# Kernel optimization log

Measured on AMD Instinct MI355X. Metric: run time of the kernel, lower is better.

Reference implementation:

```python
import jax, jax.numpy as jnp
import numpy as np

DIM = 1024
HEADS = 16
EPS = 1e-5


def layer_norm(x, gamma, beta):
    mu = jnp.mean(x, axis=-1, keepdims=True)
    var = jnp.mean(jnp.square(x - mu), axis=-1, keepdims=True)
    return (x - mu) * jax.lax.rsqrt(var + EPS) * gamma + beta


def setup_inputs() -> dict:
    key = jax.random.key(0)
    ks = jax.random.split(key, 9)
    B, Nq, Nk = 8, 1024, 1024
    s = 1.0 / np.sqrt(DIM)
    return {
        "x": jax.random.normal(ks[0], (B, Nq, DIM), jnp.float32),
        "context": jax.random.normal(ks[1], (B, Nk, DIM), jnp.float32),
        "relative_position_bias": jax.random.normal(ks[2], (HEADS, Nq, Nk), jnp.float32),
        "Wq": jax.random.normal(ks[3], (DIM, DIM), jnp.float32) * s,
        "Wk": jax.random.normal(ks[4], (DIM, DIM), jnp.float32) * s,
        "Wv": jax.random.normal(ks[5], (DIM, DIM), jnp.float32) * s,
        "Wo": jax.random.normal(ks[6], (DIM, DIM), jnp.float32) * s,
        "bo": jnp.zeros((DIM,), jnp.float32),
        "gamma": jnp.ones((DIM,), jnp.float32),
        "beta": jnp.zeros((DIM,), jnp.float32),
    }


def reference(x, context, relative_position_bias, Wq, Wk, Wv, Wo, bo, gamma, beta):
    h = HEADS
    d = DIM // h
    scale = d ** -0.5
    xn = layer_norm(x, gamma, beta)
    cn = layer_norm(context, gamma, beta)
    B, Nq, _ = x.shape
    Nk = context.shape[1]
    # b n (h d) -> b h n d
    q = (xn @ Wq).reshape(B, Nq, h, d).transpose(0, 2, 1, 3)
    k = (cn @ Wk).reshape(B, Nk, h, d).transpose(0, 2, 1, 3)
    v = (cn @ Wv).reshape(B, Nk, h, d).transpose(0, 2, 1, 3)
    scores = jnp.einsum('bhid,bhjd->bhij', q, k) * scale
    scores = scores + relative_position_bias[None]
    attn = jax.nn.softmax(scores, axis=-1)
    out = jnp.einsum('bhij,bhjd->bhid', attn, v)
    out = out.transpose(0, 2, 1, 3).reshape(B, Nq, h * d)
    return out @ Wo + bo
```

## Files before the change

### kernel.cpp

```cpp
#include <hip/hip_runtime.h>
#include <hip/hip_bf16.h>
#include <stdint.h>

#define DIM   1024
#define HEADS 16
#define HD    64
#define NB    8
#define NTOK  1024
#define MROWS (NB*NTOK)

typedef __attribute__((ext_vector_type(8))) _Float16 f16x8;
typedef __attribute__((ext_vector_type(4))) _Float16 f16x4;
typedef __attribute__((ext_vector_type(4))) float    f32x4;

typedef unsigned int uint_as1 __attribute__((address_space(1)));
typedef unsigned int uint_as3 __attribute__((address_space(3)));

__device__ __forceinline__ void gload16(const void* g, void* l) {
    __builtin_amdgcn_global_load_lds((const uint_as1*)g, (uint_as3*)l, 16, 0, 0);
}

__device__ __forceinline__ unsigned pkrtz(float a, float b) {
    auto h = __builtin_amdgcn_cvt_pkrtz(a, b);
    return __builtin_bit_cast(unsigned, h);
}

__global__ __launch_bounds__(256) void ln_kernel(const float* __restrict__ x,
                                                 const float* __restrict__ ctx,
                                                 const float* __restrict__ gamma,
                                                 const float* __restrict__ beta,
                                                 _Float16* __restrict__ xn,
                                                 _Float16* __restrict__ cn) {
    int row = blockIdx.x;
    const float* src; _Float16* dst;
    if (row < MROWS) { src = x + (size_t)row * DIM;          dst = xn + (size_t)row * DIM; }
    else             { int r = row - MROWS;
                       src = ctx + (size_t)r * DIM;          dst = cn + (size_t)r * DIM; }
    int t = threadIdx.x;
    float4 v = *(const float4*)(src + t * 4);
    float s  = v.x + v.y + v.z + v.w;
    float s2 = v.x*v.x + v.y*v.y + v.z*v.z + v.w*v.w;
    #pragma unroll
    for (int o = 32; o; o >>= 1) { s += __shfl_xor(s, o, 64); s2 += __shfl_xor(s2, o, 64); }
    __shared__ float red[8];
    int w = t >> 6, l = t & 63;
    if (l == 0) { red[w] = s; red[4 + w] = s2; }
    __syncthreads();
    s  = red[0] + red[1] + red[2] + red[3];
    s2 = red[4] + red[5] + red[6] + red[7];
    float mu   = s * (1.0f / DIM);
    float rstd = rsqrtf(s2 * (1.0f / DIM) - mu * mu + 1e-5f);
    float4 g  = *(const float4*)(gamma + t * 4);
    float4 bb = *(const float4*)(beta  + t * 4);
    f16x4 o;
    o[0] = (_Float16)((v.x - mu) * rstd * g.x + bb.x);
    o[1] = (_Float16)((v.y - mu) * rstd * g.y + bb.y);
    o[2] = (_Float16)((v.z - mu) * rstd * g.z + bb.z);
    o[3] = (_Float16)((v.w - mu) * rstd * g.w + bb.w);
    *(f16x4*)(dst + t * 4) = o;
}

__global__ __launch_bounds__(256) void wtrans_kernel(const float* __restrict__ Wq, const float* __restrict__ Wk,
                                                     const float* __restrict__ Wv, const float* __restrict__ Wo,
                                                     _Float16* __restrict__ Tq, _Float16* __restrict__ Tk,
                                                     _Float16* __restrict__ Tv, _Float16* __restrict__ To) {
    __shared__ float tile[32][33];
    int m = blockIdx.z;
    const float* W = (m == 0) ? Wq : (m == 1) ? Wk : (m == 2) ? Wv : Wo;
    _Float16*    T = (m == 0) ? Tq : (m == 1) ? Tk : (m == 2) ? Tv : To;
    int j0 = blockIdx.x * 32, k0 = blockIdx.y * 32;
    int tx = threadIdx.x, ty = threadIdx.y;
    #pragma unroll
    for (int i = 0; i < 4; i++) tile[ty + i*8][tx] = W[(size_t)(k0 + ty + i*8) * DIM + j0 + tx];
    __syncthreads();
    #pragma unroll
    for (int i = 0; i < 4; i++) T[(size_t)(j0 + ty + i*8) * DIM + k0 + tx] = (_Float16)tile[tx][ty + i*8];
}

template<int MODE>
__global__ __launch_bounds__(256) void gemm_bt(const _Float16* __restrict__ A,
                                               const _Float16* __restrict__ BT,
                                               void* __restrict__ Cout,
                                               const float* __restrict__ bias) {
    __shared__ _Float16 As[128 * 32];
    __shared__ _Float16 Bs[128 * 32];
    const int K = DIM;
    int m0 = blockIdx.x * 128, n0 = blockIdx.y * 128;
    int t = threadIdx.x, w = t >> 6, l = t & 63;
    int wr = w >> 1, wc = w & 1, ln = l & 15, qtr = l >> 4;
    f32x4 acc[4][4] = {};
    int srow = t >> 2, scol = (t & 3) * 8;
    const _Float16* Ag = A  + (size_t)(m0 + srow) * K + scol;
    const _Float16* Bg = BT + (size_t)(n0 + srow) * K + scol;
    _Float16* Al = &As[(w * 16) * 32];
    _Float16* Bl = &Bs[(w * 16) * 32];
    for (int kt = 0; kt < K; kt += 32) {
        gload16(Ag,                    Al);
        gload16(Ag + (size_t)64 * K,   Al + 64 * 32);
        gload16(Bg,                    Bl);
        gload16(Bg + (size_t)64 * K,   Bl + 64 * 32);
        Ag += 32; Bg += 32;
        __syncthreads();
        f16x8 af[4], bfr[4];
        #pragma unroll
        for (int r = 0; r < 4; r++) af[r]  = *(const f16x8*)&As[(wr * 64 + r * 16 + ln) * 32 + qtr * 8];
        #pragma unroll
        for (int c = 0; c < 4; c++) bfr[c] = *(const f16x8*)&Bs[(wc * 64 + c * 16 + ln) * 32 + qtr * 8];
        #pragma unroll
        for (int r = 0; r < 4; r++)
            #pragma unroll
            for (int c = 0; c < 4; c++)
                acc[r][c] = __builtin_amdgcn_mfma_f32_16x16x32_f16(af[r], bfr[c], acc[r][c], 0, 0, 0);
        __syncthreads();
    }
    #pragma unroll
    for (int r = 0; r < 4; r++)
        #pragma unroll
        for (int c = 0; c < 4; c++) {
            int gn = n0 + wc * 64 + c * 16 + ln;
            #pragma unroll
            for (int q = 0; q < 4; q++) {
                int gm = m0 + wr * 64 + r * 16 + qtr * 4 + q;
                float v = acc[r][c][q];
                if constexpr (MODE == 0) {
                    int b = gm >> 10, n = gm & 1023, h = gn >> 6, d = gn & 63;
                    ((_Float16*)Cout)[(((size_t)(b * HEADS + h) * NTOK + n) << 6) + d] = (_Float16)v;
                } else if constexpr (MODE == 2) {
                    int b = gm >> 10, n = gm & 1023, h = gn >> 6, d = gn & 63;
                    ((_Float16*)Cout)[(((size_t)(b * HEADS + h) * HD + d) << 10) + n] = (_Float16)v;
                } else {
                    ((float*)Cout)[(size_t)gm * DIM + gn] = v + bias[gn];
                }
            }
        }
}

__global__ __launch_bounds__(256) void attn_kernel(const _Float16* __restrict__ qb,
                                                   const _Float16* __restrict__ kb,
                                                   const _Float16* __restrict__ vt,
                                                   const float* __restrict__ bias,
                                                   _Float16* __restrict__ ao) {
    __shared__ _Float16 Kt[2][64 * 64];
    __shared__ _Float16 Vs[2][64 * 64];
    int bid = blockIdx.x;
    int id2 = (bid & 7) * 128 + (bid >> 3);
    int qt = id2 & 7, h = (id2 >> 3) & 15, b = id2 >> 7;
    int q0 = qt * 128;
    int t = threadIdx.x, w = t >> 6, l = t & 63, ln = l & 15, qtr = l >> 4;
    const _Float16* qbase = qb + (size_t)(b * HEADS + h) * NTOK * HD;
    const _Float16* kbase = kb + (size_t)(b * HEADS + h) * NTOK * HD;
    const _Float16* vbase = vt + (size_t)(b * HEADS + h) * HD * NTOK;
    const float*    bbase = bias + ((size_t)h * NTOK + q0 + w * 32) * NTOK;

    f16x8 qfr[2][2];
    #pragma unroll
    for (int qf = 0; qf < 2; qf++)
        #pragma unroll
        for (int ks = 0; ks < 2; ks++)
            qfr[qf][ks] = *(const f16x8*)&qbase[(size_t)(q0 + w*32 + qf*16 + ln) * HD + ks*32 + qtr*8];

#define STAGE(BUF, J0) do {                                                     \
        int rb_ = w * 16;                                                       \
        _Float16* kl_ = &Kt[BUF][rb_ * 64];                                     \
        _Float16* vl_ = &Vs[BUF][rb_ * 64];                                     \
        int r_ = rb_ + (l >> 3); int cg_ = (l & 7) ^ (r_ & 7);                  \
        gload16(kbase + (size_t)((J0) + r_) * HD + cg_ * 8, kl_);               \
        gload16(vbase + (size_t)r_ * NTOK + (J0) + cg_ * 8, vl_);               \
        r_ += 8; cg_ = (l & 7) ^ (r_ & 7);                                      \
        gload16(kbase + (size_t)((J0) + r_) * HD + cg_ * 8, kl_ + 8 * 64);      \
        gload16(vbase + (size_t)r_ * NTOK + (J0) + cg_ * 8, vl_ + 8 * 64);      \
    } while (0)

    STAGE(0, 0);
    __syncthreads();

    float m_run[2] = {-3.0e38f, -3.0e38f};
    float l_run[2] = {0.f, 0.f};
    f32x4 acc[2][4] = {};

    for (int tt = 0; tt < 16; tt++) {
        int cur = tt & 1;
        if (tt < 15) STAGE(cur ^ 1, (tt + 1) * 64);

        f32x4 st2[2][4] = {};
        #pragma unroll
        for (int r = 0; r < 4; r++) {
            int row = r * 16 + ln;
            #pragma unroll
            for (int ks = 0; ks < 2; ks++) {
                f16x8 kf = *(const f16x8*)&Kt[cur][row * 64 + (((qtr + ks*4) ^ (ln & 7)) * 8)];
                st2[0][r] = __builtin_amdgcn_mfma_f32_16x16x32_f16(kf, qfr[0][ks], st2[0][r], 0, 0, 0);
                st2[1][r] = __builtin_amdgcn_mfma_f32_16x16x32_f16(kf, qfr[1][ks], st2[1][r], 0, 0, 0);
            }
        }

        f16x8 pfr[2][2];
        #pragma unroll
        for (int qf = 0; qf < 2; qf++) {
            const float* bq = bbase + (size_t)(qf*16 + ln) * NTOK + tt*64 + qtr*4;
            float sv[4][4];
            float pmax = -3.0e38f;
            #pragma unroll
            for (int r = 0; r < 4; r++) {
                float4 bb = *(const float4*)(bq + r * 16);
                float s0 = st2[qf][r][0] * 0.125f + bb.x;
                float s1 = st2[qf][r][1] * 0.125f + bb.y;
                float s2 = st2[qf][r][2] * 0.125f + bb.z;
                float s3 = st2[qf][r][3] * 0.125f + bb.w;
                sv[r][0] = s0; sv[r][1] = s1; sv[r][2] = s2; sv[r][3] = s3;
                pmax = fmaxf(pmax, fmaxf(fmaxf(s0, s1), fmaxf(s2, s3)));
            }
            pmax = fmaxf(pmax, __shfl_xor(pmax, 16, 64));
            pmax = fmaxf(pmax, __shfl_xor(pmax, 32, 64));
            if (__any(pmax > m_run[qf])) {
                float mnew = fmaxf(m_run[qf], pmax);
                float f = __expf(m_run[qf] - mnew);
                m_run[qf] = mnew;
                l_run[qf] *= f;
                float fm[4];
                #pragma unroll
                for (int m = 0; m < 4; m++) fm[m] = __shfl(f, (l & 48) | (qtr * 4 + m), 64);
                #pragma unroll
                for (int dg = 0; dg < 4; dg++)
                    #pragma unroll
                    for (int m = 0; m < 4; m++) acc[qf][dg][m] *= fm[m];
            }
            float sig = 0.f;
            unsigned pk2[4][2];
            #pragma unroll
            for (int r = 0; r < 4; r++) {
                float p0 = __expf(sv[r][0] - m_run[qf]);
                float p1 = __expf(sv[r][1] - m_run[qf]);
                float p2 = __expf(sv[r][2] - m_run[qf]);
                float p3 = __expf(sv[r][3] - m_run[qf]);
                sig += (p0 + p1) + (p2 + p3);
                pk2[r][0] = pkrtz(p0, p1);
                pk2[r][1] = pkrtz(p2, p3);
            }
            sig += __shfl_xor(sig, 16, 64);
            sig += __shfl_xor(sig, 32, 64);
            l_run[qf] += sig;

            #pragma unroll
            for (int ks = 0; ks < 2; ks++) {
                unsigned pw[4];
                #pragma unroll
                for (int c = 0; c < 2; c++) {
                    unsigned X = pk2[2*ks][c], Y = pk2[2*ks + 1][c];
                    unsigned Z  = (qtr < 2) ? X : Y;
                    unsigned Wv = (qtr < 2) ? Y : X;
                    unsigned Vv = (unsigned)__shfl_xor((int)Wv, 32, 64);
                    unsigned U  = (qtr & 2) ? Vv : Z;
                    unsigned T  = (qtr & 2) ? Z : Vv;
                    unsigned sU = (unsigned)__shfl_xor((int)U, 16, 64);
                    unsigned sT = (unsigned)__shfl_xor((int)T, 16, 64);
                    pw[c]     = (qtr & 1) ? sT : U;
                    pw[2 + c] = (qtr & 1) ? T : sU;
                }
                pfr[qf][ks] = __builtin_bit_cast(f16x8, *(const uint4*)pw);
            }
        }

        #pragma unroll
        for (int dg = 0; dg < 4; dg++) {
            int row = dg * 16 + ln;
            #pragma unroll
            for (int ks = 0; ks < 2; ks++) {
                f16x8 vf = *(const f16x8*)&Vs[cur][row * 64 + (((qtr + ks*4) ^ (ln & 7)) * 8)];
                acc[0][dg] = __builtin_amdgcn_mfma_f32_16x16x32_f16(pfr[0][ks], vf, acc[0][dg], 0, 0, 0);
                acc[1][dg] = __builtin_amdgcn_mfma_f32_16x16x32_f16(pfr[1][ks], vf, acc[1][dg], 0, 0, 0);
            }
        }
        __syncthreads();
    }

    #pragma unroll
    for (int qf = 0; qf < 2; qf++) {
        float inv = 1.0f / l_run[qf];
        float invm[4];
        #pragma unroll
        for (int m = 0; m < 4; m++) invm[m] = __shfl(inv, (l & 48) | (qtr * 4 + m), 64);
        size_t rowb = (size_t)b * NTOK + q0 + w * 32 + qf * 16 + qtr * 4;
        #pragma unroll
        for (int dg = 0; dg < 4; dg++)
            #pragma unroll
            for (int m = 0; m < 4; m++)
                ao[(rowb + m) * DIM + h * HD + dg * 16 + ln] = (_Float16)(acc[qf][dg][m] * invm[m]);
    }
#undef STAGE
}

extern "C" void kernel_launch(void* const* d_in, const int* in_sizes, int n_in,
                              void* d_out, int out_size, void* d_ws, size_t ws_size,
                              hipStream_t stream) {
    const float* x     = (const float*)d_in[0];
    const float* ctx   = (const float*)d_in[1];
    const float* bias  = (const float*)d_in[2];
    const float* Wq    = (const float*)d_in[3];
    const float* Wk    = (const float*)d_in[4];
    const float* Wv    = (const float*)d_in[5];
    const float* Wo    = (const float*)d_in[6];
    const float* bo    = (const float*)d_in[7];
    const float* gamma = (const float*)d_in[8];
    const float* beta  = (const float*)d_in[9];
    float* out = (float*)d_out;

    _Float16* ws  = (_Float16*)d_ws;
    _Float16* xn  = ws;
    _Float16* cn  = xn  + (size_t)MROWS * DIM;
    _Float16* wqT = cn  + (size_t)MROWS * DIM;
    _Float16* wkT = wqT + (size_t)DIM * DIM;
    _Float16* wvT = wkT + (size_t)DIM * DIM;
    _Float16* woT = wvT + (size_t)DIM * DIM;
    _Float16* qbf = woT + (size_t)DIM * DIM;
    _Float16* kbf = qbf + (size_t)MROWS * DIM;
    _Float16* vtb = kbf + (size_t)MROWS * DIM;
    _Float16* aob = vtb + (size_t)MROWS * DIM;

    ln_kernel<<<dim3(2 * MROWS), dim3(256), 0, stream>>>(x, ctx, gamma, beta, xn, cn);
    wtrans_kernel<<<dim3(32, 32, 4), dim3(32, 8), 0, stream>>>(Wq, Wk, Wv, Wo, wqT, wkT, wvT, woT);
    gemm_bt<0><<<dim3(64, 8), dim3(256), 0, stream>>>(xn, wqT, qbf, nullptr);
    gemm_bt<0><<<dim3(64, 8), dim3(256), 0, stream>>>(cn, wkT, kbf, nullptr);
    gemm_bt<2><<<dim3(64, 8), dim3(256), 0, stream>>>(cn, wvT, vtb, nullptr);
    attn_kernel<<<dim3(NB * HEADS * 8), dim3(256), 0, stream>>>(qbf, kbf, vtb, bias, aob);
    gemm_bt<3><<<dim3(64, 8), dim3(256), 0, stream>>>(aob, woT, out, bo);
}
```

Before: 268.1 us.

## Convert bias to fp16 log2 domain, prefetch it, use exp2 and lazy rescale

```diff
diff --git a/kernel.cpp b/kernel.cpp
--- a/kernel.cpp
+++ b/kernel.cpp
@@ -8,6 +8,9 @@
 #define NB    8
 #define NTOK  1024
 #define MROWS (NB*NTOK)
+
+#define LOG2E 1.4426950408889634f
+#define SCL   (0.125f * LOG2E)
 
 typedef __attribute__((ext_vector_type(8))) _Float16 f16x8;
 typedef __attribute__((ext_vector_type(4))) _Float16 f16x4;
@@ -58,6 +61,19 @@
     o[2] = (_Float16)((v.z - mu) * rstd * g.z + bb.z);
     o[3] = (_Float16)((v.w - mu) * rstd * g.w + bb.w);
     *(f16x4*)(dst + t * 4) = o;
+}
+
+__global__ __launch_bounds__(256) void biasconv_kernel(const float* __restrict__ bias,
+                                                       _Float16* __restrict__ bias2) {
+    size_t i = ((size_t)blockIdx.x * 256 + threadIdx.x) * 8;
+    float4 a = *(const float4*)(bias + i);
+    float4 b = *(const float4*)(bias + i + 4);
+    f16x8 o;
+    o[0] = (_Float16)(a.x * LOG2E); o[1] = (_Float16)(a.y * LOG2E);
+    o[2] = (_Float16)(a.z * LOG2E); o[3] = (_Float16)(a.w * LOG2E);
+    o[4] = (_Float16)(b.x * LOG2E); o[5] = (_Float16)(b.y * LOG2E);
+    o[6] = (_Float16)(b.z * LOG2E); o[7] = (_Float16)(b.w * LOG2E);
+    *(f16x8*)(bias2 + i) = o;
 }
 
 __global__ __launch_bounds__(256) void wtrans_kernel(const float* __restrict__ Wq, const float* __restrict__ Wk,
@@ -135,11 +151,11 @@
         }
 }
 
-__global__ __launch_bounds__(256) void attn_kernel(const _Float16* __restrict__ qb,
-                                                   const _Float16* __restrict__ kb,
-                                                   const _Float16* __restrict__ vt,
-                                                   const float* __restrict__ bias,
-                                                   _Float16* __restrict__ ao) {
+__global__ __launch_bounds__(256, 4) void attn_kernel(const _Float16* __restrict__ qb,
+                                                      const _Float16* __restrict__ kb,
+                                                      const _Float16* __restrict__ vt,
+                                                      const _Float16* __restrict__ bias2,
+                                                      _Float16* __restrict__ ao) {
     __shared__ _Float16 Kt[2][64 * 64];
     __shared__ _Float16 Vs[2][64 * 64];
     int bid = blockIdx.x;
@@ -150,7 +166,7 @@
     const _Float16* qbase = qb + (size_t)(b * HEADS + h) * NTOK * HD;
     const _Float16* kbase = kb + (size_t)(b * HEADS + h) * NTOK * HD;
     const _Float16* vbase = vt + (size_t)(b * HEADS + h) * HD * NTOK;
-    const float*    bbase = bias + ((size_t)h * NTOK + q0 + w * 32) * NTOK;
+    const _Float16* bbase = bias2 + ((size_t)h * NTOK + q0 + w * 32) * NTOK;
 
     f16x8 qfr[2][2];
     #pragma unroll
@@ -171,18 +187,31 @@
         gload16(vbase + (size_t)r_ * NTOK + (J0) + cg_ * 8, vl_ + 8 * 64);      \
     } while (0)
 
+#define LOADB(DST, TT) do {                                                     \
+        _Pragma("unroll")                                                       \
+        for (int qf_ = 0; qf_ < 2; qf_++)                                       \
+            _Pragma("unroll")                                                   \
+            for (int r_ = 0; r_ < 4; r_++)                                      \
+                DST[qf_][r_] = *(const f16x4*)&bbase[(size_t)(qf_*16 + ln) * NTOK \
+                                                     + (TT)*64 + qtr*4 + r_*16]; \
+    } while (0)
+
     STAGE(0, 0);
+    f16x4 bpp[2][2][4];
+    LOADB(bpp[0], 0);
     __syncthreads();
 
     float m_run[2] = {-3.0e38f, -3.0e38f};
     float l_run[2] = {0.f, 0.f};
     f32x4 acc[2][4] = {};
 
+    #pragma unroll 2
     for (int tt = 0; tt < 16; tt++) {
         int cur = tt & 1;
-        if (tt < 15) STAGE(cur ^ 1, (tt + 1) * 64);
+        if (tt < 15) { STAGE(cur ^ 1, (tt + 1) * 64); LOADB(bpp[cur ^ 1], tt + 1); }
 
         f32x4 st2[2][4] = {};
+        __builtin_amdgcn_s_setprio(1);
         #pragma unroll
         for (int r = 0; r < 4; r++) {
             int row = r * 16 + ln;
@@ -193,28 +222,28 @@
                 st2[1][r] = __builtin_amdgcn_mfma_f32_16x16x32_f16(kf, qfr[1][ks], st2[1][r], 0, 0, 0);
             }
         }
+        __builtin_amdgcn_s_setprio(0);
 
         f16x8 pfr[2][2];
         #pragma unroll
         for (int qf = 0; qf < 2; qf++) {
-            const float* bq = bbase + (size_t)(qf*16 + ln) * NTOK + tt*64 + qtr*4;
             float sv[4][4];
             float pmax = -3.0e38f;
             #pragma unroll
             for (int r = 0; r < 4; r++) {
-                float4 bb = *(const float4*)(bq + r * 16);
-                float s0 = st2[qf][r][0] * 0.125f + bb.x;
-                float s1 = st2[qf][r][1] * 0.125f + bb.y;
-                float s2 = st2[qf][r][2] * 0.125f + bb.z;
-                float s3 = st2[qf][r][3] * 0.125f + bb.w;
+                f16x4 bb = bpp[cur][qf][r];
+                float s0 = fmaf(st2[qf][r][0], SCL, (float)bb[0]);
+                float s1 = fmaf(st2[qf][r][1], SCL, (float)bb[1]);
+                float s2 = fmaf(st2[qf][r][2], SCL, (float)bb[2]);
+                float s3 = fmaf(st2[qf][r][3], SCL, (float)bb[3]);
                 sv[r][0] = s0; sv[r][1] = s1; sv[r][2] = s2; sv[r][3] = s3;
                 pmax = fmaxf(pmax, fmaxf(fmaxf(s0, s1), fmaxf(s2, s3)));
             }
             pmax = fmaxf(pmax, __shfl_xor(pmax, 16, 64));
             pmax = fmaxf(pmax, __shfl_xor(pmax, 32, 64));
-            if (__any(pmax > m_run[qf])) {
+            if (!__all(pmax <= m_run[qf] + 8.f)) {
                 float mnew = fmaxf(m_run[qf], pmax);
-                float f = __expf(m_run[qf] - mnew);
+                float f = exp2f(m_run[qf] - mnew);
                 m_run[qf] = mnew;
                 l_run[qf] *= f;
                 float fm[4];
@@ -229,10 +258,10 @@
             unsigned pk2[4][2];
             #pragma unroll
             for (int r = 0; r < 4; r++) {
-                float p0 = __expf(sv[r][0] - m_run[qf]);
-                float p1 = __expf(sv[r][1] - m_run[qf]);
-                float p2 = __expf(sv[r][2] - m_run[qf]);
-                float p3 = __expf(sv[r][3] - m_run[qf]);
+                float p0 = exp2f(sv[r][0] - m_run[qf]);
+                float p1 = exp2f(sv[r][1] - m_run[qf]);
+                float p2 = exp2f(sv[r][2] - m_run[qf]);
+                float p3 = exp2f(sv[r][3] - m_run[qf]);
                 sig += (p0 + p1) + (p2 + p3);
                 pk2[r][0] = pkrtz(p0, p1);
                 pk2[r][1] = pkrtz(p2, p3);
@@ -261,6 +290,7 @@
             }
         }
 
+        __builtin_amdgcn_s_setprio(1);
         #pragma unroll
         for (int dg = 0; dg < 4; dg++) {
             int row = dg * 16 + ln;
@@ -271,6 +301,7 @@
                 acc[1][dg] = __builtin_amdgcn_mfma_f32_16x16x32_f16(pfr[1][ks], vf, acc[1][dg], 0, 0, 0);
             }
         }
+        __builtin_amdgcn_s_setprio(0);
         __syncthreads();
     }
 
@@ -288,6 +319,7 @@
                 ao[(rowb + m) * DIM + h * HD + dg * 16 + ln] = (_Float16)(acc[qf][dg][m] * invm[m]);
     }
 #undef STAGE
+#undef LOADB
 }
 
 extern "C" void kernel_launch(void* const* d_in, const int* in_sizes, int n_in,
@@ -316,12 +348,14 @@
     _Float16* kbf = qbf + (size_t)MROWS * DIM;
     _Float16* vtb = kbf + (size_t)MROWS * DIM;
     _Float16* aob = vtb + (size_t)MROWS * DIM;
+    _Float16* bias2 = ws;
 
     ln_kernel<<<dim3(2 * MROWS), dim3(256), 0, stream>>>(x, ctx, gamma, beta, xn, cn);
     wtrans_kernel<<<dim3(32, 32, 4), dim3(32, 8), 0, stream>>>(Wq, Wk, Wv, Wo, wqT, wkT, wvT, woT);
     gemm_bt<0><<<dim3(64, 8), dim3(256), 0, stream>>>(xn, wqT, qbf, nullptr);
     gemm_bt<0><<<dim3(64, 8), dim3(256), 0, stream>>>(cn, wkT, kbf, nullptr);
     gemm_bt<2><<<dim3(64, 8), dim3(256), 0, stream>>>(cn, wvT, vtb, nullptr);
-    attn_kernel<<<dim3(NB * HEADS * 8), dim3(256), 0, stream>>>(qbf, kbf, vtb, bias, aob);
+    biasconv_kernel<<<dim3(8192), dim3(256), 0, stream>>>(bias, bias2);
+    attn_kernel<<<dim3(NB * HEADS * 8), dim3(256), 0, stream>>>(qbf, kbf, vtb, bias2, aob);
     gemm_bt<3><<<dim3(64, 8), dim3(256), 0, stream>>>(aob, woT, out, bo);
 }
```

Result: slower. 289.8 us (+8.1%).
